# Kernel tuning notes

Hardware: AMD Instinct MI355X
Metric: run time of the kernel (lower is better)

## Reference

```python
import jax, jax.numpy as jnp
import numpy as np
import math

H = 12      # num_heads
DH = 64     # head_dim
NEG = -1e30 # masked logit value
M_TRUNC = 2 # poisson_trunc


def _rotate_half(x):
    d = x.shape[-1] // 2
    return jnp.concatenate([-x[..., d:], x[..., :d]], axis=-1)


def setup_inputs() -> dict:
    key = jax.random.key(0)
    k0, k1, k2 = jax.random.split(key, 3)
    B, T, C = 1, 4096, 768
    x = jax.random.normal(k0, (B, T, C), jnp.float32)
    W_qkv = jax.random.normal(k1, (C, 3 * C), jnp.float32) * (C ** -0.5)
    W_proj = jax.random.normal(k2, (C, C), jnp.float32) * (C ** -0.5)
    # standard RoPE tables, concat layout matching rotate_half
    inv_freq = 1.0 / (10000.0 ** (jnp.arange(0, DH, 2, dtype=jnp.float32) / DH))
    ang = jnp.arange(T, dtype=jnp.float32)[:, None] * inv_freq[None, :]  # [T, DH/2]
    cos = jnp.concatenate([jnp.cos(ang), jnp.cos(ang)], axis=-1)  # [T, DH]
    sin = jnp.concatenate([jnp.sin(ang), jnp.sin(ang)], axis=-1)
    dt_logit = jnp.float32(math.log(0.999 / (1.0 - 0.999)))            # sigmoid -> 0.999
    kappa_uncon = jnp.float32(math.log(math.expm1(1.0) + 1e-8))        # softplus -> 1.0
    xi_uncon = jnp.float32(math.log(math.expm1(32.0) + 1e-8))          # softplus -> 32.0
    return dict(x=x, cos=cos, sin=sin, W_qkv=W_qkv, W_proj=W_proj,
                dt_logit=dt_logit, kappa_uncon=kappa_uncon, xi_uncon=xi_uncon)


def reference(x, cos, sin, W_qkv, W_proj, dt_logit, kappa_uncon, xi_uncon):
    B, T, C = x.shape
    qkv = x @ W_qkv                         # [B,T,3C]
    q, k, v = jnp.split(qkv, 3, axis=-1)
    split_heads = lambda t: t.reshape(B, T, H, DH).transpose(0, 2, 1, 3)  # [B,H,T,Dh]
    q, k, v = split_heads(q), split_heads(k), split_heads(v)
    c, s = cos[None, None], sin[None, None]
    q = q * c + _rotate_half(q) * s
    k = k * c + _rotate_half(k) * s
    dp = jnp.einsum('bhtd,bhsd->bhts', q, k) / math.sqrt(DH)  # [B,H,T,T]
    kappa = jax.nn.softplus(kappa_uncon)
    xi = jax.nn.softplus(xi_uncon)
    idx = jnp.arange(T)
    dist = (idx[:, None] - idx[None, :]).astype(jnp.float32)
    prior = -kappa * (dist / xi) ** 2       # Gaussian diffusion prior
    allowed = idx[:, None] >= idx[None, :]  # causal tril
    logits = jnp.where(allowed[None, None], dp + prior[None, None], NEG)
    P = jax.nn.softmax(logits, axis=-1)     # row-stochastic Markov kernel
    # truncated, renormalized Poisson mixture of matrix powers: exp(t(P-I)) v
    dt = jax.nn.sigmoid(dt_logit)
    w = jnp.stack([dt ** m * jnp.exp(-dt) / math.factorial(m) for m in range(M_TRUNC + 1)])
    w = w / jnp.sum(w)
    y = w[0] * v
    pv = v
    for m in range(1, M_TRUNC + 1):         # fixed small iteration count
        pv = jnp.einsum('bhts,bhsd->bhtd', P, pv)
        y = y + w[m] * pv
    y = y.transpose(0, 2, 1, 3).reshape(B, T, C)
    return y @ W_proj
```

## Files before the change

kernel.cpp:

```cpp
#include <hip/hip_runtime.h>
#include <hip/hip_bf16.h>

#define Tn 4096
#define Cn 768
#define Hn 12
#define DHn 64
#define BAND 192
#define QBLK 64
#define TJ 256
#define NTW 13

typedef __attribute__((ext_vector_type(8))) short short8;
typedef __attribute__((ext_vector_type(4))) short short4v;
typedef __attribute__((ext_vector_type(4))) float f32x4;

__device__ __forceinline__ float b2f(unsigned short u) {
  union { unsigned int i; float f; } z; z.i = ((unsigned int)u) << 16; return z.f;
}
__device__ __forceinline__ unsigned short f2b(float f) {
  union { float f; unsigned int i; } z; z.f = f;
  unsigned int r = z.i + 0x7FFFu + ((z.i >> 16) & 1u);
  return (unsigned short)(r >> 16);
}

__global__ __launch_bounds__(256) void k_prep(const float* __restrict__ x,
                                              unsigned short* __restrict__ x_bf,
                                              const float* __restrict__ Wqkv,
                                              unsigned short* __restrict__ WqkvT,
                                              const float* __restrict__ Wproj,
                                              unsigned short* __restrict__ WprojT) {
  __shared__ float tile[32][33];
  int b = blockIdx.x, tid = threadIdx.x;
  if (b < 512) {
    int n4 = Tn * Cn / 4;
    for (int i = b * 256 + tid; i < n4; i += 512 * 256) {
      float4 v = ((const float4*)x)[i];
      short4v o;
      o.x = (short)f2b(v.x); o.y = (short)f2b(v.y);
      o.z = (short)f2b(v.z); o.w = (short)f2b(v.w);
      ((short4v*)x_bf)[i] = o;
    }
    return;
  }
  const float* W; unsigned short* WT; int N, r;
  if (b < 2240) { r = b - 512; W = Wqkv; WT = WqkvT; N = 3 * Cn; }
  else          { r = b - 2240; W = Wproj; WT = WprojT; N = Cn; }
  int nb = N / 32;
  int n0 = (r % nb) * 32, k0 = (r / nb) * 32;
  int tx = tid & 31, ty = tid >> 5;
  for (int rr = ty; rr < 32; rr += 8) tile[rr][tx] = W[(size_t)(k0 + rr) * N + n0 + tx];
  __syncthreads();
  for (int rr = ty; rr < 32; rr += 8) WT[(size_t)(n0 + rr) * Cn + k0 + tx] = f2b(tile[tx][rr]);
}


template<int ROWS, int NTHR>
__device__ __forceinline__ void stage_mat(const unsigned short* __restrict__ Gb,
                                          int K, unsigned short* buf, int k0, int tid) {
  constexpr int CHUNKS = ROWS * 8;
#pragma unroll
  for (int it = 0; it < CHUNKS / NTHR; ++it) {
    int c = it * NTHR + tid;
    int row = c >> 3;
    int kc = (c & 7) ^ (row & 7);
    const unsigned short* ga = Gb + (size_t)row * K + k0 + kc * 8;
    __builtin_amdgcn_global_load_lds((const __attribute__((address_space(1))) void*)ga,
                                     (__attribute__((address_space(3))) void*)(buf + c * 8),
                                     16, 0, 0);
  }
}

__device__ __forceinline__ short8 frag_read64(const unsigned short* buf, int row, int q) {
  int s = q ^ (row & 7);
  return *(const short8*)(buf + row * 64 + s * 8);
}

__global__ __launch_bounds__(256, 3) void k_gqkv(const unsigned short* __restrict__ A,
                                                 const unsigned short* __restrict__ BT,
                                                 const float* __restrict__ cosT,
                                                 const float* __restrict__ sinT,
                                                 unsigned short* __restrict__ qout,
                                                 unsigned short* __restrict__ kout,
                                                 unsigned short* __restrict__ vout) {
  __shared__ __align__(16) unsigned short Ls[2][12288];
  int tid = threadIdx.x, lane = tid & 63, wave = tid >> 6;
  int lq = lane & 15, g = (lane >> 4) & 3;
  int wr = wave >> 1, wc = wave & 1;
  int nx = gridDim.x;
  int nwg = nx * gridDim.y;
  int lid = blockIdx.y * nx + blockIdx.x;
  int swz = (lid & 7) * (nwg >> 3) + (lid >> 3);
  int bx = swz % nx, by = swz / nx;
  int m0 = by * 64, n0 = bx * 128;
  const unsigned short* Ab = A + (size_t)m0 * Cn;
  const unsigned short* Bb = BT + (size_t)n0 * Cn;
  f32x4 acc[2][4] = {};
  const int NK = Cn >> 6;
  stage_mat<64, 256>(Ab, Cn, Ls[0], 0, tid);
  stage_mat<128, 256>(Bb, Cn, Ls[0] + 4096, 0, tid);
  stage_mat<64, 256>(Ab, Cn, Ls[1], 64, tid);
  stage_mat<128, 256>(Bb, Cn, Ls[1] + 4096, 64, tid);
  for (int kt = 0; kt < NK; ++kt) {
    if (kt + 1 < NK) asm volatile("s_waitcnt vmcnt(6)" ::: "memory");
    else             asm volatile("s_waitcnt vmcnt(0)" ::: "memory");
    __builtin_amdgcn_s_barrier();
    __builtin_amdgcn_sched_barrier(0);
    const unsigned short* Ac = Ls[kt & 1];
    const unsigned short* Bc = Ls[kt & 1] + 4096;
#pragma unroll
    for (int kk = 0; kk < 2; ++kk) {
      short8 a[2], b[4];
#pragma unroll
      for (int m = 0; m < 2; ++m) a[m] = frag_read64(Ac, wr * 32 + m * 16 + lq, kk * 4 + g);
#pragma unroll
      for (int n = 0; n < 4; ++n) b[n] = frag_read64(Bc, wc * 64 + n * 16 + lq, kk * 4 + g);
#pragma unroll
      for (int m = 0; m < 2; ++m)
#pragma unroll
        for (int n = 0; n < 4; ++n)
          acc[m][n] = __builtin_amdgcn_mfma_f32_16x16x32_bf16(a[m], b[n], acc[m][n], 0, 0, 0);
    }
    __builtin_amdgcn_sched_barrier(0);
    __builtin_amdgcn_s_barrier();
    if (kt + 2 < NK) {
      stage_mat<64, 256>(Ab, Cn, Ls[kt & 1], (kt + 2) << 6, tid);
      stage_mat<128, 256>(Bb, Cn, Ls[kt & 1] + 4096, (kt + 2) << 6, tid);
    }
  }
  __syncthreads();
  int col0 = n0 + wc * 64;
  int part = col0 / Cn;
  unsigned short* Lo = (unsigned short*)Ls;
#pragma unroll
  for (int m = 0; m < 2; ++m)
#pragma unroll
    for (int i = 0; i < 4; ++i) {
      int lr = wr * 32 + m * 16 + g * 4 + i;
      int t = m0 + lr;
#pragma unroll
      for (int n = 0; n < 4; ++n) {
        int d = n * 16 + lq;
        float val = acc[m][n][i];
        if (part < 2) {
          float cv = cosT[t * DHn + d], sv = sinT[t * DHn + d];
          float partner = acc[m][n ^ 2][i];
          val = (n < 2) ? fmaf(-partner, sv, val * cv) : fmaf(partner, sv, val * cv);
        }
        Lo[lr * 128 + wc * 64 + d] = f2b(val);
      }
    }
  __syncthreads();
#pragma unroll
  for (int it = 0; it < 4; ++it) {
    int c = it * 256 + tid;
    int tr = c >> 4, cc = c & 15;
    int cola = n0 + (cc << 3);
    int pp = cola / Cn;
    int h = (cola % Cn) / DHn;
    int d0 = cola % DHn;
    unsigned short* dst = pp == 0 ? qout : (pp == 1 ? kout : vout);
    *(short8*)(dst + ((size_t)h * Tn + (m0 + tr)) * DHn + d0) = *(const short8*)(Lo + tr * 128 + (cc << 3));
  }
}

__global__ __launch_bounds__(256, 4) void k_gproj(const unsigned short* __restrict__ A,
                                                  const unsigned short* __restrict__ BT,
                                                  float* __restrict__ Cout) {
  __shared__ __align__(16) unsigned short Ls[2][8192];
  int tid = threadIdx.x, lane = tid & 63, wave = tid >> 6;
  int lq = lane & 15, g = (lane >> 4) & 3;
  int wr = wave >> 1, wc = wave & 1;
  int nx = gridDim.x;
  int nwg = nx * gridDim.y;
  int lid = blockIdx.y * nx + blockIdx.x;
  int swz = (lid & 7) * (nwg >> 3) + (lid >> 3);
  int bx = swz % nx, by = swz / nx;
  int m0 = by * 64, n0 = bx * 64;
  const unsigned short* Ab = A + (size_t)m0 * Cn;
  const unsigned short* Bb = BT + (size_t)n0 * Cn;
  f32x4 acc[2][2] = {};
  const int NK = Cn >> 6;
  stage_mat<64, 256>(Ab, Cn, Ls[0], 0, tid);
  stage_mat<64, 256>(Bb, Cn, Ls[0] + 4096, 0, tid);
  stage_mat<64, 256>(Ab, Cn, Ls[1], 64, tid);
  stage_mat<64, 256>(Bb, Cn, Ls[1] + 4096, 64, tid);
  for (int kt = 0; kt < NK; ++kt) {
    if (kt + 1 < NK) asm volatile("s_waitcnt vmcnt(4)" ::: "memory");
    else             asm volatile("s_waitcnt vmcnt(0)" ::: "memory");
    __builtin_amdgcn_s_barrier();
    __builtin_amdgcn_sched_barrier(0);
    const unsigned short* Ac = Ls[kt & 1];
    const unsigned short* Bc = Ls[kt & 1] + 4096;
#pragma unroll
    for (int kk = 0; kk < 2; ++kk) {
      short8 a[2], b[2];
#pragma unroll
      for (int m = 0; m < 2; ++m) a[m] = frag_read64(Ac, wr * 32 + m * 16 + lq, kk * 4 + g);
#pragma unroll
      for (int n = 0; n < 2; ++n) b[n] = frag_read64(Bc, wc * 32 + n * 16 + lq, kk * 4 + g);
#pragma unroll
      for (int m = 0; m < 2; ++m)
#pragma unroll
        for (int n = 0; n < 2; ++n)
          acc[m][n] = __builtin_amdgcn_mfma_f32_16x16x32_bf16(a[m], b[n], acc[m][n], 0, 0, 0);
    }
    __builtin_amdgcn_sched_barrier(0);
    __builtin_amdgcn_s_barrier();
    if (kt + 2 < NK) {
      stage_mat<64, 256>(Ab, Cn, Ls[kt & 1], (kt + 2) << 6, tid);
      stage_mat<64, 256>(Bb, Cn, Ls[kt & 1] + 4096, (kt + 2) << 6, tid);
    }
  }
  int r0 = m0 + wr * 32 + g * 4;
  int c0 = n0 + wc * 32 + lq;
#pragma unroll
  for (int m = 0; m < 2; ++m)
#pragma unroll
    for (int n = 0; n < 2; ++n)
#pragma unroll
      for (int i = 0; i < 2 * 2; ++i)
        Cout[(size_t)(r0 + m * 16 + i) * Cn + c0 + n * 16] = acc[m][n][i];
}

__device__ __forceinline__ void stage_subtiled(const unsigned short* __restrict__ srcHead,
                                               int jt0, unsigned short* lds, int tid, int wave) {
#pragma unroll
  for (int it = 0; it < 8; ++it) {
    int c = it * 256 + tid;
    int j = jt0 + ((c >> 5) << 2) + ((c & 7) >> 1);
    j = j < 0 ? 0 : j;
    int d0 = (((c >> 3) & 3) << 4) + ((c & 1) << 3);
    const unsigned short* ga = srcHead + (size_t)j * DHn + d0;
    __builtin_amdgcn_global_load_lds((const __attribute__((address_space(1))) void*)ga,
                                     (__attribute__((address_space(3))) void*)(lds + (it * 4 + wave) * 512),
                                     16, 0, 0);
  }
}

__device__ __forceinline__ void pv_tr(const unsigned short* Vt, const short8* af,
                                      int wave, int lane, f32x4* oacc) {
  int lq = lane & 15, g = lane >> 4;
  unsigned base = (unsigned)(size_t)(const __attribute__((address_space(3))) unsigned short*)Vt;
  unsigned pl = base + lq * 8;
#pragma unroll
  for (int e = 0; e < 7; ++e) {
    int kl = 16 * wave + 32 * e + 8 * g;
    if (kl > TJ - 8) kl = TJ - 8;
    unsigned pe = pl + kl * 128;
    unsigned long long rr[8];
#pragma unroll
    for (int dt = 0; dt < 4; ++dt) {
      asm volatile("ds_read_b64_tr_b16 %0, %1" : "=v"(rr[2 * dt]) : "v"(pe + dt * 128));
      asm volatile("ds_read_b64_tr_b16 %0, %1" : "=v"(rr[2 * dt + 1]) : "v"(pe + dt * 128 + 512));
    }
    asm volatile("s_waitcnt lgkmcnt(0)");
    __builtin_amdgcn_sched_barrier(0);
#pragma unroll
    for (int dt = 0; dt < 4; ++dt) {
      union { unsigned long long u[2]; short8 s; } vb;
      vb.u[0] = rr[2 * dt]; vb.u[1] = rr[2 * dt + 1];
      oacc[dt] = __builtin_amdgcn_mfma_f32_16x16x32_bf16(af[e], vb.s, oacc[dt], 0, 0, 0);
    }
  }
}

__global__ __launch_bounds__(256) void k_attn_a(const unsigned short* __restrict__ qr,
                                                const unsigned short* __restrict__ kr,
                                                const unsigned short* __restrict__ vin,
                                                unsigned short* __restrict__ pv1out,
                                                unsigned short* __restrict__ pfrag,
                                                const float* __restrict__ kap_p,
                                                const float* __restrict__ xi_p) {
  __shared__ unsigned short Ks[TJ * DHn];
  __shared__ unsigned short Vt[TJ * DHn];
  int tid = threadIdx.x, lane = tid & 63, wave = tid >> 6;
  int lq = lane & 15, g = lane >> 4;
  int i0 = blockIdx.x * QBLK, h = blockIdx.y;
  int jt0 = i0 - BAND;
  const size_t headoff = (size_t)h * Tn * DHn;

  const unsigned short* krh = kr + headoff;
#pragma unroll
  for (int it = 0; it < 8; ++it) {
    int u = it * 256 + tid;
    int row = u >> 3, c8 = u & 7;
    int j = jt0 + row; j = j < 0 ? 0 : j;
    const unsigned short* ga = krh + (size_t)j * DHn + ((c8 ^ (row & 7)) << 3);
    __builtin_amdgcn_global_load_lds((const __attribute__((address_space(1))) void*)ga,
                                     (__attribute__((address_space(3))) void*)((char*)Ks + (size_t)(it * 256 + wave * 64) * 16),
                                     16, 0, 0);
  }
  stage_subtiled(vin + headoff, jt0, Vt, tid, wave);

  const unsigned short* qrh = qr + headoff;
  int q0 = i0 + wave * 16;
  short8 qf0 = *(const short8*)(qrh + (size_t)(q0 + lq) * DHn + g * 8);
  short8 qf1 = *(const short8*)(qrh + (size_t)(q0 + lq) * DHn + 32 + g * 8);
  __syncthreads();

  f32x4 st[NTW];
#pragma unroll
  for (int t = 0; t < NTW; ++t) st[t] = (f32x4){0.f, 0.f, 0.f, 0.f};
#pragma unroll
  for (int t = 0; t < NTW; ++t) {
    int row = (wave + t) * 16 + lq;
    const char* kb = (const char*)Ks + row * 128;
    int sw = row & 7;
    short8 ka0 = *(const short8*)(kb + ((g ^ sw) << 4));
    short8 ka1 = *(const short8*)(kb + (((4 + g) ^ sw) << 4));
    st[t] = __builtin_amdgcn_mfma_f32_16x16x32_bf16(ka0, qf0, st[t], 0, 0, 0);
    st[t] = __builtin_amdgcn_mfma_f32_16x16x32_bf16(ka1, qf1, st[t], 0, 0, 0);
  }

  float kap = log1pf(__expf(*kap_p));
  float xi  = log1pf(__expf(*xi_p));
  const float LOG2E = 1.4426950408889634f;
  float sc = 0.125f * LOG2E;
  float c2 = kap / (xi * xi) * LOG2E;
  float db0 = (float)(lq + BAND - 4 * g);
  float jb0 = (float)(jt0 + 16 * wave + 4 * g);
  float m = -3.0e38f;
#pragma unroll
  for (int t = 0; t < NTW; ++t) {
#pragma unroll
    for (int r = 0; r < 4; ++r) {
      float off = (float)(16 * t + r);
      float dist = db0 - off;
      float jv = jb0 + off;
      float l2 = fmaf(dist * dist, -c2, st[t][r] * sc);
      bool bad = (dist < 0.f) || (jv < 0.f);
      l2 = bad ? -3.0e38f : l2;
      st[t][r] = l2;
      m = fmaxf(m, l2);
    }
  }
  m = fmaxf(m, __shfl_xor(m, 16));
  m = fmaxf(m, __shfl_xor(m, 32));
  float sum = 0.f;
#pragma unroll
  for (int t = 0; t < NTW; ++t) {
#pragma unroll
    for (int r = 0; r < 4; ++r) {
      float p = exp2f(st[t][r] - m);
      st[t][r] = p;
      sum += p;
    }
  }
  sum += __shfl_xor(sum, 16);
  sum += __shfl_xor(sum, 32);
  float inv_s = 1.f / sum;

  unsigned int pk0[NTW], pk1[NTW];
#pragma unroll
  for (int t = 0; t < NTW; ++t) {
    pk0[t] = (unsigned int)f2b(st[t][0] * inv_s) | ((unsigned int)f2b(st[t][1] * inv_s) << 16);
    pk1[t] = (unsigned int)f2b(st[t][2] * inv_s) | ((unsigned int)f2b(st[t][3] * inv_s) << 16);
  }

  short8 af[7];
  int srcA = lq + (g & 1) * 32;
  int srcB = srcA + 16;
  bool hiT = (g >= 2);
#pragma unroll
  for (int e = 0; e < 7; ++e) {
    unsigned int aA0 = __shfl(pk0[2 * e], srcA);
    unsigned int aA1 = __shfl(pk1[2 * e], srcA);
    unsigned int aB0 = __shfl(pk0[2 * e], srcB);
    unsigned int aB1 = __shfl(pk1[2 * e], srcB);
    unsigned int dw0, dw1, dw2, dw3;
    if (e < 6) {
      unsigned int bA0 = __shfl(pk0[2 * e + 1], srcA);
      unsigned int bA1 = __shfl(pk1[2 * e + 1], srcA);
      unsigned int bB0 = __shfl(pk0[2 * e + 1], srcB);
      unsigned int bB1 = __shfl(pk1[2 * e + 1], srcB);
      dw0 = hiT ? bA0 : aA0; dw1 = hiT ? bA1 : aA1;
      dw2 = hiT ? bB0 : aB0; dw3 = hiT ? bB1 : aB1;
    } else {
      dw0 = hiT ? 0u : aA0; dw1 = hiT ? 0u : aA1;
      dw2 = hiT ? 0u : aB0; dw3 = hiT ? 0u : aB1;
    }
    union { unsigned int u[4]; short8 s; } t2;
    t2.u[0] = dw0; t2.u[1] = dw1; t2.u[2] = dw2; t2.u[3] = dw3;
    af[e] = t2.s;
  }

  size_t pfb = ((((size_t)h * (Tn / QBLK) + blockIdx.x) * 4 + wave) * 7) * 512 + (size_t)lane * 8;
#pragma unroll
  for (int e = 0; e < 7; ++e)
    *(short8*)(pfrag + pfb + (size_t)e * 512) = af[e];

  f32x4 oacc[4];
#pragma unroll
  for (int dt = 0; dt < 4; ++dt) oacc[dt] = (f32x4){0.f, 0.f, 0.f, 0.f};
  pv_tr(Vt, af, wave, lane, oacc);

#pragma unroll
  for (int dt = 0; dt < 4; ++dt)
#pragma unroll
    for (int r = 0; r < 4; ++r) {
      int i = i0 + 16 * wave + 4 * g + r;
      pv1out[headoff + (size_t)i * DHn + dt * 16 + lq] = f2b(oacc[dt][r]);
    }
}

__global__ __launch_bounds__(256) void k_attn_b(const unsigned short* __restrict__ pv1,
                                                const unsigned short* __restrict__ v0,
                                                const unsigned short* __restrict__ pfrag,
                                                unsigned short* __restrict__ yout,
                                                const float* __restrict__ dt_logit_p) {
  __shared__ unsigned short Vt[TJ * DHn];
  int tid = threadIdx.x, lane = tid & 63, wave = tid >> 6;
  int lq = lane & 15, g = lane >> 4;
  int i0 = blockIdx.x * QBLK, h = blockIdx.y;
  int jt0 = i0 - BAND;
  const size_t headoff = (size_t)h * Tn * DHn;

  stage_subtiled(pv1 + headoff, jt0, Vt, tid, wave);

  short8 af[7];
  size_t pfb = ((((size_t)h * (Tn / QBLK) + blockIdx.x) * 4 + wave) * 7) * 512 + (size_t)lane * 8;
#pragma unroll
  for (int e = 0; e < 7; ++e)
    af[e] = *(const short8*)(pfrag + pfb + (size_t)e * 512);
  __syncthreads();

  f32x4 oacc[4];
#pragma unroll
  for (int dt = 0; dt < 4; ++dt) oacc[dt] = (f32x4){0.f, 0.f, 0.f, 0.f};
  pv_tr(Vt, af, wave, lane, oacc);

  float dtv = 1.f / (1.f + __expf(-*dt_logit_p));
  float a1 = dtv, a2 = 0.5f * dtv * dtv;
  float inv3 = 1.f / (1.f + a1 + a2);
  float w0 = inv3, w1 = a1 * inv3, w2 = a2 * inv3;

#pragma unroll
  for (int dt = 0; dt < 4; ++dt)
#pragma unroll
    for (int r = 0; r < 4; ++r) {
      int i = i0 + 16 * wave + 4 * g + r;
      int j = 192 + 16 * wave + 4 * g + r;
      unsigned boff = (unsigned)((j >> 2) * 512 + dt * 128 + (j & 3) * 32 + lq * 2);
      float p1 = b2f(*(const unsigned short*)((const char*)Vt + boff));
      float vv = b2f(v0[headoff + (size_t)i * DHn + dt * 16 + lq]);
      float yv = w0 * vv + w1 * p1 + w2 * oacc[dt][r];
      yout[(size_t)i * Cn + h * DHn + dt * 16 + lq] = f2b(yv);
    }
}

extern "C" void kernel_launch(void* const* d_in, const int* in_sizes, int n_in,
                              void* d_out, int out_size, void* d_ws, size_t ws_size,
                              hipStream_t stream) {
  (void)in_sizes; (void)n_in; (void)out_size; (void)ws_size;
  const float* x     = (const float*)d_in[0];
  const float* cosT  = (const float*)d_in[1];
  const float* sinT  = (const float*)d_in[2];
  const float* Wqkv  = (const float*)d_in[3];
  const float* Wproj = (const float*)d_in[4];
  const float* dtl   = (const float*)d_in[5];
  const float* kap   = (const float*)d_in[6];
  const float* xiu   = (const float*)d_in[7];
  float* out = (float*)d_out;
  char* ws = (char*)d_ws;
  size_t off = 0;
  auto alloc = [&](size_t bytes) { char* p = ws + off; off += (bytes + 255) & ~(size_t)255; return p; };
  unsigned short* x_bf   = (unsigned short*)alloc((size_t)Tn * Cn * 2);
  unsigned short* WqkvT  = (unsigned short*)alloc((size_t)3 * Cn * Cn * 2);
  unsigned short* WprojT = (unsigned short*)alloc((size_t)Cn * Cn * 2);
  unsigned short* q_r    = (unsigned short*)alloc((size_t)Hn * Tn * DHn * 2);
  unsigned short* k_r    = (unsigned short*)alloc((size_t)Hn * Tn * DHn * 2);
  unsigned short* v_s    = (unsigned short*)alloc((size_t)Hn * Tn * DHn * 2);
  unsigned short* pv1    = (unsigned short*)alloc((size_t)Hn * Tn * DHn * 2);
  unsigned short* y_bf   = (unsigned short*)alloc((size_t)Tn * Cn * 2);
  unsigned short* pfrag  = (unsigned short*)alloc((size_t)Hn * (Tn / QBLK) * 4 * 7 * 512 * 2);

  k_prep<<<2816, 256, 0, stream>>>(x, x_bf, Wqkv, WqkvT, Wproj, WprojT);
  k_gqkv<<<dim3(3 * Cn / 128, Tn / 64), 256, 0, stream>>>(
      x_bf, WqkvT, cosT, sinT, q_r, k_r, v_s);
  k_attn_a<<<dim3(Tn / QBLK, Hn), 256, 0, stream>>>(q_r, k_r, v_s, pv1, pfrag, kap, xiu);
  k_attn_b<<<dim3(Tn / QBLK, Hn), 256, 0, stream>>>(pv1, v_s, pfrag, y_bf, dtl);
  k_gproj<<<dim3(Cn / 64, Tn / 64), 256, 0, stream>>>(y_bf, WprojT, out);
}
```

Before: 83.90 us.

## Reuse K shared buffer for V in attention kernel to halve LDS

The first attention kernel now stages K into two 128-row shared buffers, computes the QK scores, then overwrites the same buffers with V, instead of holding separate K and V tiles. Halving LDS per block should allow more resident blocks per CU. V loading is also deferred so it overlaps with the softmax and fragment-packing work. The cost is an extra barrier, a serialized dependency between the K use and the V load, and some added address selection in the inner loops.

```diff
diff --git a/kernel.cpp b/kernel.cpp
--- a/kernel.cpp
+++ b/kernel.cpp
@@ -52,7 +52,6 @@
   __syncthreads();
   for (int rr = ty; rr < 32; rr += 8) WT[(size_t)(n0 + rr) * Cn + k0 + tx] = f2b(tile[tx][rr]);
 }
-
 
 template<int ROWS, int NTHR>
 __device__ __forceinline__ void stage_mat(const unsigned short* __restrict__ Gb,
@@ -237,6 +236,21 @@
   }
 }
 
+__device__ __forceinline__ void stage_half_sub(const unsigned short* __restrict__ srcHead,
+                                               int jbase, unsigned short* buf, int tid) {
+#pragma unroll
+  for (int it = 0; it < 4; ++it) {
+    int cc = it * 256 + tid;
+    int j = jbase + ((cc >> 5) << 2) + ((cc & 7) >> 1);
+    j = j < 0 ? 0 : j;
+    int d0 = (((cc >> 3) & 3) << 4) + ((cc & 1) << 3);
+    const unsigned short* ga = srcHead + (size_t)j * DHn + d0;
+    __builtin_amdgcn_global_load_lds((const __attribute__((address_space(1))) void*)ga,
+                                     (__attribute__((address_space(3))) void*)(buf + cc * 8),
+                                     16, 0, 0);
+  }
+}
+
 __device__ __forceinline__ void pv_tr(const unsigned short* Vt, const short8* af,
                                       int wave, int lane, f32x4* oacc) {
   int lq = lane & 15, g = lane >> 4;
@@ -247,6 +261,35 @@
     int kl = 16 * wave + 32 * e + 8 * g;
     if (kl > TJ - 8) kl = TJ - 8;
     unsigned pe = pl + kl * 128;
+    unsigned long long rr[8];
+#pragma unroll
+    for (int dt = 0; dt < 4; ++dt) {
+      asm volatile("ds_read_b64_tr_b16 %0, %1" : "=v"(rr[2 * dt]) : "v"(pe + dt * 128));
+      asm volatile("ds_read_b64_tr_b16 %0, %1" : "=v"(rr[2 * dt + 1]) : "v"(pe + dt * 128 + 512));
+    }
+    asm volatile("s_waitcnt lgkmcnt(0)");
+    __builtin_amdgcn_sched_barrier(0);
+#pragma unroll
+    for (int dt = 0; dt < 4; ++dt) {
+      union { unsigned long long u[2]; short8 s; } vb;
+      vb.u[0] = rr[2 * dt]; vb.u[1] = rr[2 * dt + 1];
+      oacc[dt] = __builtin_amdgcn_mfma_f32_16x16x32_bf16(af[e], vb.s, oacc[dt], 0, 0, 0);
+    }
+  }
+}
+
+__device__ __forceinline__ void pv_tr2(const unsigned short* V0h, const unsigned short* V1h,
+                                       const short8* af, int wave, int lane, f32x4* oacc) {
+  int lq = lane & 15, g = lane >> 4;
+  unsigned b0 = (unsigned)(size_t)(const __attribute__((address_space(3))) unsigned short*)V0h;
+  unsigned b1 = (unsigned)(size_t)(const __attribute__((address_space(3))) unsigned short*)V1h;
+#pragma unroll
+  for (int e = 0; e < 7; ++e) {
+    int kl = 16 * wave + 32 * e + 8 * g;
+    if (kl > TJ - 8) kl = TJ - 8;
+    unsigned base = (kl < 128) ? b0 : b1;
+    int klo = kl & 127;
+    unsigned pe = base + lq * 8 + klo * 128;
     unsigned long long rr[8];
 #pragma unroll
     for (int dt = 0; dt < 4; ++dt) {
@@ -271,8 +314,8 @@
                                                 unsigned short* __restrict__ pfrag,
                                                 const float* __restrict__ kap_p,
                                                 const float* __restrict__ xi_p) {
-  __shared__ unsigned short Ks[TJ * DHn];
-  __shared__ unsigned short Vt[TJ * DHn];
+  __shared__ __align__(16) unsigned short B0[128 * DHn];
+  __shared__ __align__(16) unsigned short B1[128 * DHn];
   int tid = threadIdx.x, lane = tid & 63, wave = tid >> 6;
   int lq = lane & 15, g = lane >> 4;
   int i0 = blockIdx.x * QBLK, h = blockIdx.y;
@@ -282,21 +325,22 @@
   const unsigned short* krh = kr + headoff;
 #pragma unroll
   for (int it = 0; it < 8; ++it) {
-    int u = it * 256 + tid;
-    int row = u >> 3, c8 = u & 7;
-    int j = jt0 + row; j = j < 0 ? 0 : j;
+    int c = it * 256 + tid;
+    int half = c >> 10, cc = c & 1023;
+    int row = cc >> 3, c8 = cc & 7;
+    int j = jt0 + half * 128 + row; j = j < 0 ? 0 : j;
     const unsigned short* ga = krh + (size_t)j * DHn + ((c8 ^ (row & 7)) << 3);
     __builtin_amdgcn_global_load_lds((const __attribute__((address_space(1))) void*)ga,
-                                     (__attribute__((address_space(3))) void*)((char*)Ks + (size_t)(it * 256 + wave * 64) * 16),
+                                     (__attribute__((address_space(3))) void*)((half ? B1 : B0) + cc * 8),
                                      16, 0, 0);
   }
-  stage_subtiled(vin + headoff, jt0, Vt, tid, wave);
 
   const unsigned short* qrh = qr + headoff;
   int q0 = i0 + wave * 16;
   short8 qf0 = *(const short8*)(qrh + (size_t)(q0 + lq) * DHn + g * 8);
   short8 qf1 = *(const short8*)(qrh + (size_t)(q0 + lq) * DHn + 32 + g * 8);
-  __syncthreads();
+  asm volatile("s_waitcnt vmcnt(0)" ::: "memory");
+  __builtin_amdgcn_s_barrier();
 
   f32x4 st[NTW];
 #pragma unroll
@@ -304,13 +348,19 @@
 #pragma unroll
   for (int t = 0; t < NTW; ++t) {
     int row = (wave + t) * 16 + lq;
-    const char* kb = (const char*)Ks + row * 128;
+    const char* kb = (row < 128) ? ((const char*)B0 + row * 128)
+                                 : ((const char*)B1 + (row - 128) * 128);
     int sw = row & 7;
     short8 ka0 = *(const short8*)(kb + ((g ^ sw) << 4));
     short8 ka1 = *(const short8*)(kb + (((4 + g) ^ sw) << 4));
     st[t] = __builtin_amdgcn_mfma_f32_16x16x32_bf16(ka0, qf0, st[t], 0, 0, 0);
     st[t] = __builtin_amdgcn_mfma_f32_16x16x32_bf16(ka1, qf1, st[t], 0, 0, 0);
   }
+  __syncthreads();
+
+  const unsigned short* vrh = vin + headoff;
+  stage_half_sub(vrh, jt0, B0, tid);
+  stage_half_sub(vrh, jt0 + 128, B1, tid);
 
   float kap = log1pf(__expf(*kap_p));
   float xi  = log1pf(__expf(*xi_p));
@@ -389,10 +439,12 @@
   for (int e = 0; e < 7; ++e)
     *(short8*)(pfrag + pfb + (size_t)e * 512) = af[e];
 
+  asm volatile("s_waitcnt vmcnt(0)" ::: "memory");
+  __builtin_amdgcn_s_barrier();
   f32x4 oacc[4];
 #pragma unroll
   for (int dt = 0; dt < 4; ++dt) oacc[dt] = (f32x4){0.f, 0.f, 0.f, 0.f};
-  pv_tr(Vt, af, wave, lane, oacc);
+  pv_tr2(B0, B1, af, wave, lane, oacc);
 
 #pragma unroll
   for (int dt = 0; dt < 4; ++dt)
```

Result: faster. 81.66 us (-2.7%).
